# Performance work log

Hardware: AMD Instinct MI355X
Metric: run time of the kernel (lower is better)

The kernel has to match this reference:

```python
import jax, jax.numpy as jnp
import numpy as np

V, E, H = 32000, 256, 512
B, S, T = 32, 80, 80


def setup_inputs() -> dict:
    key = jax.random.key(0)
    ks = jax.random.split(key, 16)
    s = 0.05
    emb = jax.random.normal(ks[0], (V, E), jnp.float32) * s
    emb = emb.at[0].set(0.0)  # padding_idx=0 row is zero
    inp = {
        "src": jax.random.randint(ks[1], (B, S), 0, V),
        "tgt": jax.random.randint(ks[2], (B, T), 0, V),
        "emb": emb,
        "enc_Wih": jax.random.normal(ks[3], (3 * H, E), jnp.float32) * s,
        "enc_Whh": jax.random.normal(ks[4], (3 * H, H), jnp.float32) * s,
        "enc_bih": jax.random.normal(ks[5], (3 * H,), jnp.float32) * s,
        "enc_bhh": jax.random.normal(ks[6], (3 * H,), jnp.float32) * s,
        "dec_Wih": jax.random.normal(ks[7], (3 * H, E), jnp.float32) * s,
        "dec_Whh": jax.random.normal(ks[8], (3 * H, H), jnp.float32) * s,
        "dec_bih": jax.random.normal(ks[9], (3 * H,), jnp.float32) * s,
        "dec_bhh": jax.random.normal(ks[10], (3 * H,), jnp.float32) * s,
        "out_W": jax.random.normal(ks[11], (V, 2 * H), jnp.float32) * s,
        "out_b": jax.random.normal(ks[12], (V,), jnp.float32) * s,
    }
    return inp


def _gru_cell(x, h, Wih, Whh, bih, bhh):
    # PyTorch GRU cell: gates ordered (r, z, n)
    gi = x @ Wih.T + bih          # (B, 3H)
    gh = h @ Whh.T + bhh          # (B, 3H)
    i_r, i_z, i_n = jnp.split(gi, 3, axis=-1)
    h_r, h_z, h_n = jnp.split(gh, 3, axis=-1)
    r = jax.nn.sigmoid(i_r + h_r)
    z = jax.nn.sigmoid(i_z + h_z)
    n = jnp.tanh(i_n + r * h_n)
    return (1.0 - z) * n + z * h


def reference(src, tgt, emb, enc_Wih, enc_Whh, enc_bih, enc_bhh,
              dec_Wih, dec_Whh, dec_bih, dec_bhh, out_W, out_b):
    Bsz, Tlen = tgt.shape

    # ---- encoder: single-layer GRU over src ----
    x_src = emb[src]                              # (B, S, E)
    h0 = jnp.zeros((Bsz, H), x_src.dtype)

    def enc_step(h, x_t):
        h = _gru_cell(x_t, h, enc_Wih, enc_Whh, enc_bih, enc_bhh)
        return h, h

    h_enc, enc_outs = jax.lax.scan(enc_step, h0, jnp.swapaxes(x_src, 0, 1))
    enc_outs = jnp.swapaxes(enc_outs, 0, 1)       # (B, S, H)

    # ---- decoder: teacher forcing (ratio=1.0), steps t=1..T-1 ----
    x_dec = emb[tgt[:, :-1]]                      # (B, T-1, E)

    def dec_step(h, x_t):
        h = _gru_cell(x_t, h, dec_Wih, dec_Whh, dec_bih, dec_bhh)
        # Luong dot attention on new hidden state
        scores = jnp.einsum('bsh,bh->bs', enc_outs, h)
        aw = jax.nn.softmax(scores, axis=1)
        ctx = jnp.einsum('bs,bsh->bh', aw, enc_outs)
        combined = jnp.concatenate([h, ctx], axis=1)   # (B, 2H)
        step_logits = combined @ out_W.T + out_b       # (B, V)
        return h, step_logits

    _, step_logits = jax.lax.scan(dec_step, h_enc, jnp.swapaxes(x_dec, 0, 1))
    step_logits = jnp.swapaxes(step_logits, 0, 1)      # (B, T-1, V)

    # logits[:, 0, :] stays zero, matching the torch module
    logits = jnp.concatenate(
        [jnp.zeros((Bsz, 1, V), step_logits.dtype), step_logits], axis=1)
    return logits
```

## Files before the change

### kernel.cpp

```cpp
#include <hip/hip_runtime.h>

#define VV 32000
#define EE 256
#define HH 512
#define BB 32
#define SS 80
#define TT 80

typedef __attribute__((ext_vector_type(8))) _Float16 half8;
typedef __attribute__((ext_vector_type(4))) _Float16 half4;
typedef __attribute__((ext_vector_type(4))) float floatx4;
typedef unsigned long long u64;

__device__ __forceinline__ void gload16(const _Float16* g, _Float16* l) {
  __builtin_amdgcn_global_load_lds((const __attribute__((address_space(1))) void*)g,
                                   (__attribute__((address_space(3))) void*)l, 16, 0, 0);
}

__device__ __forceinline__ u64 aload(const u64* p) {
  return __hip_atomic_load(p, __ATOMIC_RELAXED, __HIP_MEMORY_SCOPE_AGENT);
}
__device__ __forceinline__ void astore(u64* p, u64 v) {
  __hip_atomic_store(p, v, __ATOMIC_RELAXED, __HIP_MEMORY_SCOPE_AGENT);
}

__device__ __forceinline__ unsigned pack15(unsigned short u) {
  return (u & 0x3FFFu) | ((u >> 1) & 0x4000u);
}
__device__ __forceinline__ unsigned short unpack15(unsigned v) {
  return (unsigned short)((v & 0x3FFFu) | ((v & 0x4000u) << 1));
}
__device__ __forceinline__ u64 unpack_word4(u64 a) {
  u64 o = 0;
#pragma unroll
  for (int i = 0; i < 4; ++i)
    o |= (u64)unpack15((unsigned)(a >> (15*i)) & 0x7FFFu) << (16*i);
  return o;
}

__device__ __forceinline__ float dot8(half8 a, half8 b, float c) {
  typedef __attribute__((ext_vector_type(2))) _Float16 half2v;
  half2v a0 = {a[0],a[1]}, a1 = {a[2],a[3]}, a2 = {a[4],a[5]}, a3 = {a[6],a[7]};
  half2v b0 = {b[0],b[1]}, b1 = {b[2],b[3]}, b2 = {b[4],b[5]}, b3 = {b[6],b[7]};
  c = __builtin_amdgcn_fdot2(a0, b0, c, false);
  c = __builtin_amdgcn_fdot2(a1, b1, c, false);
  c = __builtin_amdgcn_fdot2(a2, b2, c, false);
  c = __builtin_amdgcn_fdot2(a3, b3, c, false);
  return c;
}

__device__ __forceinline__ float sigm(float x) { return 1.f/(1.f + __expf(-x)); }
__device__ __forceinline__ float tanh_f(float x) { return 2.f/(1.f + __expf(-2.f*x)) - 1.f; }

__global__ __launch_bounds__(256) void giE_direct(
    const int* __restrict__ src, const float* __restrict__ emb,
    const float* __restrict__ Wih, const float* __restrict__ bih,
    float* __restrict__ gi)
{
  __shared__ _Float16 As[4096];
  __shared__ _Float16 Bs[4096];
  const int tid = threadIdx.x;
  const int lane = tid & 63;
  const int wv = tid >> 6;
  const int wr = wv >> 1, wc = wv & 1;
  const int mt = blockIdx.y, nt = blockIdx.x;
  floatx4 acc[4][4];
#pragma unroll
  for (int i=0;i<4;++i)
#pragma unroll
    for (int j=0;j<4;++j) acc[i][j] = (floatx4){0.f,0.f,0.f,0.f};
  const int r2 = tid >> 1, cb = (tid & 1) * 16;
  const int tok = src[mt*128 + r2];
  const float* arow = emb + (size_t)tok*EE;
  const float* brow = Wih + (size_t)(nt*128 + r2)*EE;
  const int g8 = (lane >> 4) * 8;
  const int lr = lane & 15;
  for (int kb = 0; kb < EE; kb += 32) {
    __syncthreads();
#pragma unroll
    for (int q = 0; q < 4; ++q) {
      const floatx4 va = *(const floatx4*)(arow + kb + cb + q*4);
      const floatx4 vb = *(const floatx4*)(brow + kb + cb + q*4);
#pragma unroll
      for (int e = 0; e < 4; ++e) {
        As[r2*32 + cb + q*4 + e] = (_Float16)va[e];
        Bs[r2*32 + cb + q*4 + e] = (_Float16)vb[e];
      }
    }
    __syncthreads();
    half8 af[4], bf[4];
#pragma unroll
    for (int i=0;i<4;++i) af[i] = *(const half8*)(As + (wr*64 + i*16 + lr)*32 + g8);
#pragma unroll
    for (int j=0;j<4;++j) bf[j] = *(const half8*)(Bs + (wc*64 + j*16 + lr)*32 + g8);
#pragma unroll
    for (int i=0;i<4;++i)
#pragma unroll
      for (int j=0;j<4;++j)
        acc[i][j] = __builtin_amdgcn_mfma_f32_16x16x32_f16(af[i], bf[j], acc[i][j], 0,0,0);
  }
  const int rm = 4*(lane>>4);
#pragma unroll
  for (int i=0;i<4;++i)
#pragma unroll
    for (int r=0;r<4;++r) {
      const int row = mt*128 + wr*64 + i*16 + rm + r;
#pragma unroll
      for (int j=0;j<4;++j) {
        const int col = nt*128 + wc*64 + j*16 + lr;
        gi[(size_t)row*1536 + col] = acc[i][j][r] + bih[col];
      }
    }
}

__global__ __launch_bounds__(256) void giD_direct(
    const int* __restrict__ tgt, const float* __restrict__ emb,
    const float* __restrict__ Wih, const float* __restrict__ bih,
    float* __restrict__ gi)
{
  __shared__ _Float16 As[4096];
  __shared__ _Float16 Bs[4096];
  const int tid = threadIdx.x;
  const int lane = tid & 63;
  const int wv = tid >> 6;
  const int wr = wv >> 1, wc = wv & 1;
  const int mt = blockIdx.y, nt = blockIdx.x;
  floatx4 acc[4][4];
#pragma unroll
  for (int i=0;i<4;++i)
#pragma unroll
    for (int j=0;j<4;++j) acc[i][j] = (floatx4){0.f,0.f,0.f,0.f};
  const int r2 = tid >> 1, cb = (tid & 1) * 16;
  const int R = mt*128 + r2;
  int tok = -1;
  if (R < 2528) { const int b_ = R/79, tt = R - b_*79; tok = tgt[b_*80 + tt]; }
  const float* arow = (tok >= 0) ? emb + (size_t)tok*EE : nullptr;
  const float* brow = Wih + (size_t)(nt*128 + r2)*EE;
  const int g8 = (lane >> 4) * 8;
  const int lr = lane & 15;
  for (int kb = 0; kb < EE; kb += 32) {
    __syncthreads();
    if (arow) {
#pragma unroll
      for (int q = 0; q < 4; ++q) {
        const floatx4 va = *(const floatx4*)(arow + kb + cb + q*4);
#pragma unroll
        for (int e = 0; e < 4; ++e) As[r2*32 + cb + q*4 + e] = (_Float16)va[e];
      }
    } else {
#pragma unroll
      for (int q = 0; q < 16; ++q) As[r2*32 + cb + q] = (_Float16)0.f;
    }
#pragma unroll
    for (int q = 0; q < 4; ++q) {
      const floatx4 vb = *(const floatx4*)(brow + kb + cb + q*4);
#pragma unroll
      for (int e = 0; e < 4; ++e) Bs[r2*32 + cb + q*4 + e] = (_Float16)vb[e];
    }
    __syncthreads();
    half8 af[4], bf[4];
#pragma unroll
    for (int i=0;i<4;++i) af[i] = *(const half8*)(As + (wr*64 + i*16 + lr)*32 + g8);
#pragma unroll
    for (int j=0;j<4;++j) bf[j] = *(const half8*)(Bs + (wc*64 + j*16 + lr)*32 + g8);
#pragma unroll
    for (int i=0;i<4;++i)
#pragma unroll
      for (int j=0;j<4;++j)
        acc[i][j] = __builtin_amdgcn_mfma_f32_16x16x32_f16(af[i], bf[j], acc[i][j], 0,0,0);
  }
  const int rm = 4*(lane>>4);
#pragma unroll
  for (int i=0;i<4;++i)
#pragma unroll
    for (int r=0;r<4;++r) {
      const int row = mt*128 + wv ? 0 : 0, dummy = 0; (void)dummy;
    }
#pragma unroll
  for (int i=0;i<4;++i)
#pragma unroll
    for (int r=0;r<4;++r) {
      const int row = mt*128 + wr*64 + i*16 + rm + r;
      if (row < 2528) {
#pragma unroll
        for (int j=0;j<4;++j) {
          const int col = nt*128 + wc*64 + j*16 + lr;
          gi[(size_t)row*1536 + col] = acc[i][j][r] + bih[col];
        }
      }
    }
}

__global__ __launch_bounds__(256) void oWh_conv(
    const float* __restrict__ ow, _Float16* __restrict__ owh)
{
  const long total8 = (long)VV*1024/8;
  for (long i = (long)blockIdx.x*256 + threadIdx.x; i < total8; i += (long)gridDim.x*256) {
    const float* s_ = ow + i*8;
    const floatx4 a = *(const floatx4*)s_;
    const floatx4 b = *(const floatx4*)(s_ + 4);
    half8 h;
    h[0]=(_Float16)a[0]; h[1]=(_Float16)a[1]; h[2]=(_Float16)a[2]; h[3]=(_Float16)a[3];
    h[4]=(_Float16)b[0]; h[5]=(_Float16)b[1]; h[6]=(_Float16)b[2]; h[7]=(_Float16)b[3];
    *(half8*)(owh + i*8) = h;
  }
}

__global__ __launch_bounds__(256) void logits_gemm(
    const _Float16* __restrict__ A, const _Float16* __restrict__ Bm,
    const float* __restrict__ bias, float* __restrict__ out)
{
  const int p = blockIdx.x;
  const int x = p & 7, s = p >> 3;
  const int nt = x + 8*(s / 20);
  const int mt = s % 20;
  if (nt >= 250) return;
  __shared__ _Float16 As[4096];
  __shared__ _Float16 Bs[4096];
  const int tid = threadIdx.x;
  const int lane = tid & 63;
  const int wv = tid >> 6;
  const int wr = wv >> 1, wc = wv & 1;
  floatx4 acc[4][4];
#pragma unroll
  for (int i=0;i<4;++i)
#pragma unroll
    for (int j=0;j<4;++j) acc[i][j] = (floatx4){0.f,0.f,0.f,0.f};
  const int srow = lane >> 2;
  const int scol = (lane & 3) * 8;
  const _Float16* Ab = A + (size_t)(mt*128)*1024;
  const _Float16* Bb = Bm + (size_t)(nt*128)*1024;
  const int g8 = (lane >> 4) * 8;
  const int lr = lane & 15;
  for (int kb = 0; kb < 1024; kb += 32) {
    __syncthreads();
#pragma unroll
    for (int cc = 0; cc < 2; ++cc) {
      const int c = wv*2 + cc;
      gload16(Ab + (size_t)(c*16 + srow)*1024 + kb + scol, As + c*512);
      gload16(Bb + (size_t)(c*16 + srow)*1024 + kb + scol, Bs + c*512);
    }
    __syncthreads();
    half8 af[4], bf[4];
#pragma unroll
    for (int i=0;i<4;++i) af[i] = *(const half8*)(As + (wr*64 + i*16 + lr)*32 + g8);
#pragma unroll
    for (int j=0;j<4;++j) bf[j] = *(const half8*)(Bs + (wc*64 + j*16 + lr)*32 + g8);
#pragma unroll
    for (int i=0;i<4;++i)
#pragma unroll
      for (int j=0;j<4;++j)
        acc[i][j] = __builtin_amdgcn_mfma_f32_16x16x32_f16(af[i], bf[j], acc[i][j], 0,0,0);
  }
  const int rm = 4*(lane>>4);
#pragma unroll
  for (int i=0;i<4;++i)
#pragma unroll
    for (int r=0;r<4;++r) {
      const int row = mt*128 + wr*64 + i*16 + rm + r;
#pragma unroll
      for (int j=0;j<4;++j) {
        const int col = nt*128 + wc*64 + j*16 + lr;
        if (row < 2528) {
          const int b = row / 79;
          const int t = row - b*79;
          out[(size_t)(b*80 + t + 1)*VV + col] = acc[i][j][r] + bias[col];
        } else {
          out[(size_t)((row - 2528)*80)*VV + col] = 0.f;
        }
      }
    }
}

#define SEQ_SMEM (80*512*2 + 512*2 + 512*2 + 3*64*8*4 + 2*80*4)
__global__ __launch_bounds__(512) void seq_pb(
    const float* __restrict__ eWhh, const float* __restrict__ dWhh,
    const float* __restrict__ ebhh, const float* __restrict__ dbhh,
    const float* __restrict__ giE, const float* __restrict__ giD,
    u64* __restrict__ hx,
    _Float16* __restrict__ comb)
{
  extern __shared__ char smem[];
  _Float16* eo_l = (_Float16*)smem;
  _Float16* hbuf = eo_l + 80*512;
  _Float16* hatt = hbuf + 512;
  float* part = (float*)(hatt + 512);
  float* sc = part + 3*64*8;
  float* aw = sc + 80;

  const int bi = blockIdx.x;
  const int q = bi >> 5, b = bi & 31;
  const int tid = threadIdx.x;
  const int lane = tid & 63;
  const int wv = tid >> 6;
  const int jl = tid & 63;
  const int kq = tid >> 6;
  const int j  = q*64 + jl;

  half8 wreg[3][8];
  auto loadW = [&](const float* W){
#pragma unroll
    for (int g = 0; g < 3; ++g)
#pragma unroll
      for (int c = 0; c < 8; ++c) {
        const float* s8 = W + ((size_t)(g*512 + j))*512 + kq*64 + c*8;
        const floatx4 a = *(const floatx4*)s8;
        const floatx4 d = *(const floatx4*)(s8 + 4);
        half8 h;
        h[0]=(_Float16)a[0]; h[1]=(_Float16)a[1]; h[2]=(_Float16)a[2]; h[3]=(_Float16)a[3];
        h[4]=(_Float16)d[0]; h[5]=(_Float16)d[1]; h[6]=(_Float16)d[2]; h[7]=(_Float16)d[3];
        wreg[g][c] = h;
      }
  };

  auto consume = [&](int slotR, u64 rtag){
    if (tid < 112) {
      const int m = tid + (tid >= q*16 ? 16 : 0);
      const u64* sp = hx + (size_t)slotR*4096 + b*128 + m;
      u64 v = aload(sp);
      int guard = 0;
      while ((v >> 60) != rtag && guard < (1<<22)) { v = aload(sp); ++guard; }
      *(u64*)&hbuf[m*4] = unpack_word4(v);
    }
    __syncthreads();
  };
  auto publish = [&](int slotW, u64 wtag){
    if (tid < 16) {
      const int m = q*16 + tid;
      u64 wq = wtag << 60;
#pragma unroll
      for (int e = 0; e < 4; ++e) {
        union { _Float16 h; unsigned short u; } cv; cv.h = hbuf[m*4 + e];
        wq |= (u64)pack15(cv.u) << (15*e);
      }
      astore(hx + (size_t)slotW*4096 + b*128 + m, wq);
    }
  };

  float hp = 0.f;
  auto gru = [&](float gr_, float gz_, float gn_, float bR, float bZ, float bN){
    half8 hv[8];
#pragma unroll
    for (int c = 0; c < 8; ++c) hv[c] = *(const half8*)&hbuf[kq*64 + c*8];
    float p0 = 0.f, p1 = 0.f, p2 = 0.f;
#pragma unroll
    for (int c = 0; c < 8; ++c) {
      p0 = dot8(wreg[0][c], hv[c], p0);
      p1 = dot8(wreg[1][c], hv[c], p1);
      p2 = dot8(wreg[2][c], hv[c], p2);
    }
    part[(0*64 + jl)*8 + kq] = p0;
    part[(1*64 + jl)*8 + kq] = p1;
    part[(2*64 + jl)*8 + kq] = p2;
    __syncthreads();
    if (tid < 64) {
      float a0 = 0.f, a1 = 0.f, a2 = 0.f;
#pragma unroll
      for (int e = 0; e < 8; ++e) {
        a0 += part[(0*64 + tid)*8 + e];
        a1 += part[(1*64 + tid)*8 + e];
        a2 += part[(2*64 + tid)*8 + e];
      }
      const float rg = sigm(gr_ + a0 + bR);
      const float zg = sigm(gz_ + a1 + bZ);
      const float ng = tanh_f(gn_ + rg*(a2 + bN));
      const float hn = (1.f - zg)*ng + zg*hp;
      hp = hn;
      hbuf[q*64 + tid] = (_Float16)hn;
    }
    __syncthreads();
  };

  auto attention = [&](int trow){
    const half8 hf = *(const half8*)&hatt[lane*8];
#pragma unroll 2
    for (int i = 0; i < 10; ++i) {
      const int s = wv*10 + i;
      const half8 ev = *(const half8*)&eo_l[s*512 + lane*8];
      float pt = dot8(ev, hf, 0.f);
#pragma unroll
      for (int o = 32; o; o >>= 1) pt += __shfl_xor(pt, o);
      if (lane == 0) sc[s] = pt;
    }
    __syncthreads();
    if (wv == 0) {
      const float v0 = sc[lane];
      const float v1 = (lane < 16) ? sc[64+lane] : -1e30f;
      float m = fmaxf(v0, v1);
#pragma unroll
      for (int o = 32; o; o >>= 1) m = fmaxf(m, __shfl_xor(m, o));
      const float e0 = __expf(v0 - m);
      const float e1 = (lane < 16) ? __expf(v1 - m) : 0.f;
      float ssum = e0 + e1;
#pragma unroll
      for (int o = 32; o; o >>= 1) ssum += __shfl_xor(ssum, o);
      const float inv = 1.f/ssum;
      aw[lane] = e0*inv;
      if (lane < 16) aw[64+lane] = e1*inv;
    }
    __syncthreads();
    if (tid < 64) {
      float c = 0.f;
#pragma unroll 8
      for (int s = 0; s < SS; ++s) c += aw[s] * (float)eo_l[s*512 + q*64 + tid];
      _Float16* cr = comb + ((size_t)b*79 + trow)*1024;
      cr[q*64 + tid]       = hatt[q*64 + tid];
      cr[512 + q*64 + tid] = (_Float16)c;
    }
    __syncthreads();
  };

  if (tid < 128) *(u64*)&hbuf[tid*4] = 0ull;
  loadW(eWhh);
  float ebR=0.f, ebZ=0.f, ebN=0.f, dbR=0.f, dbZ=0.f, dbN=0.f;
  if (tid < 64) {
    ebR = ebhh[j]; ebZ = ebhh[512+j]; ebN = ebhh[1024+j];
    dbR = dbhh[j]; dbZ = dbhh[512+j]; dbN = dbhh[1024+j];
  }
  __syncthreads();

  for (int k = 0; k < SS; ++k) {
    float gr_=0.f, gz_=0.f, gn_=0.f;
    if (tid < 64) {
      const float* gi = giE + ((size_t)b*SS + k)*1536;
      gr_ = gi[j]; gz_ = gi[512+j]; gn_ = gi[1024+j];
    }
    consume(k & 1, (u64)(k & 15));
    if (k > 0 && tid < 128)
      *(u64*)&eo_l[(k-1)*512 + tid*4] = *(const u64*)&hbuf[tid*4];
    gru(gr_, gz_, gn_, ebR, ebZ, ebN);
    publish((k+1) & 1, (u64)((k+1) & 15));
  }

  loadW(dWhh);

  for (int t = 0; t < TT-1; ++t) {
    const int k = 80 + t;
    float gr_=0.f, gz_=0.f, gn_=0.f;
    if (tid < 64) {
      const float* gi = giD + ((size_t)b*79 + t)*1536;
      gr_ = gi[j]; gz_ = gi[512+j]; gn_ = gi[1024+j];
    }
    consume(k & 1, (u64)(k & 15));
    if (tid < 128) {
      if (t == 0) *(u64*)&eo_l[79*512 + tid*4] = *(const u64*)&hbuf[tid*4];
      else        *(u64*)&hatt[tid*4]          = *(const u64*)&hbuf[tid*4];
    }
    gru(gr_, gz_, gn_, dbR, dbZ, dbN);
    publish((k+1) & 1, (u64)((k+1) & 15));
    if (t > 0) attention(t-1);
  }

  if (tid < 112) {
    const int m = tid + (tid >= q*16 ? 16 : 0);
    const u64* sp = hx + (size_t)4096 + b*128 + m;
    u64 v = aload(sp);
    int guard = 0;
    while ((v >> 60) != 15ull && guard < (1<<22)) { v = aload(sp); ++guard; }
    *(u64*)&hbuf[m*4] = unpack_word4(v);
  }
  __syncthreads();
  if (tid < 128) *(u64*)&hatt[tid*4] = *(const u64*)&hbuf[tid*4];
  __syncthreads();
  attention(TT-2);
}

extern "C" void kernel_launch(void* const* d_in, const int* in_sizes, int n_in,
                              void* d_out, int out_size, void* d_ws, size_t ws_size,
                              hipStream_t stream) {
  (void)in_sizes; (void)n_in; (void)out_size; (void)ws_size;
  const int*   src  = (const int*)d_in[0];
  const int*   tgt  = (const int*)d_in[1];
  const float* emb  = (const float*)d_in[2];
  const float* eWih = (const float*)d_in[3];
  const float* eWhh = (const float*)d_in[4];
  const float* ebih = (const float*)d_in[5];
  const float* ebhh = (const float*)d_in[6];
  const float* dWih = (const float*)d_in[7];
  const float* dWhh = (const float*)d_in[8];
  const float* dbih = (const float*)d_in[9];
  const float* dbhh = (const float*)d_in[10];
  const float* outW = (const float*)d_in[11];
  const float* outb = (const float*)d_in[12];
  float* out = (float*)d_out;

  char* p = (char*)d_ws;
  auto alloc = [&](size_t n){ char* r = p; p += (n + 255) & ~(size_t)255; return r; };
  _Float16* oWh  = (_Float16*)alloc((size_t)VV*1024*2);
  float*    giE  = (float*)alloc((size_t)2560*1536*4);
  float*    giD  = (float*)alloc((size_t)2560*1536*4);
  u64*      hx   = (u64*)alloc((size_t)2*32*128*8);
  _Float16* comb = (_Float16*)alloc((size_t)2560*1024*2);

  hipMemsetAsync(hx, 0, (size_t)2*32*128*8, stream);
  giE_direct<<<dim3(12,20), 256, 0, stream>>>(src, emb, eWih, ebih, giE);
  giD_direct<<<dim3(12,20), 256, 0, stream>>>(tgt, emb, dWih, dbih, giD);
  oWh_conv<<<1024, 256, 0, stream>>>(outW, oWh);
  hipFuncSetAttribute((const void*)seq_pb,
                      hipFuncAttributeMaxDynamicSharedMemorySize, SEQ_SMEM);
  seq_pb<<<256, 512, SEQ_SMEM, stream>>>(eWhh, dWhh, ebhh, dbhh, giE, giD,
                                         hx, comb);
  logits_gemm<<<5120, 256, 0, stream>>>(comb, oWh, outb, out);
}
```

Measured before the change: 986.7 us.

## Fuse input-gate GEMMs and convert output weights to fp16 inside logits GEMM

Merges the encoder and decoder input-projection GEMMs into one launch with a 24x20 grid, and removes the separate fp32-to-fp16 conversion pass over the output weight matrix. The logits GEMM now loads fp32 weight rows directly and converts them into shared memory, so the 64MB-read and 64MB-write conversion pass is gone. The cost is that each logits tile reads fp32 weights, which doubles B-operand traffic across the 20 M-tiles that reuse each weight tile. It also drops the async global-to-LDS load for the B operand in favour of a register staging path.

```diff
diff --git a/kernel.cpp b/kernel.cpp
--- a/kernel.cpp
+++ b/kernel.cpp
@@ -52,10 +52,12 @@
 __device__ __forceinline__ float sigm(float x) { return 1.f/(1.f + __expf(-x)); }
 __device__ __forceinline__ float tanh_f(float x) { return 2.f/(1.f + __expf(-2.f*x)) - 1.f; }
 
-__global__ __launch_bounds__(256) void giE_direct(
-    const int* __restrict__ src, const float* __restrict__ emb,
-    const float* __restrict__ Wih, const float* __restrict__ bih,
-    float* __restrict__ gi)
+__global__ __launch_bounds__(256) void gi_fused(
+    const int* __restrict__ src, const int* __restrict__ tgt,
+    const float* __restrict__ emb,
+    const float* __restrict__ eWih, const float* __restrict__ ebih,
+    const float* __restrict__ dWih, const float* __restrict__ dbih,
+    float* __restrict__ giE, float* __restrict__ giD)
 {
   __shared__ _Float16 As[4096];
   __shared__ _Float16 Bs[4096];
@@ -63,68 +65,12 @@
   const int lane = tid & 63;
   const int wv = tid >> 6;
   const int wr = wv >> 1, wc = wv & 1;
-  const int mt = blockIdx.y, nt = blockIdx.x;
-  floatx4 acc[4][4];
-#pragma unroll
-  for (int i=0;i<4;++i)
-#pragma unroll
-    for (int j=0;j<4;++j) acc[i][j] = (floatx4){0.f,0.f,0.f,0.f};
-  const int r2 = tid >> 1, cb = (tid & 1) * 16;
-  const int tok = src[mt*128 + r2];
-  const float* arow = emb + (size_t)tok*EE;
-  const float* brow = Wih + (size_t)(nt*128 + r2)*EE;
-  const int g8 = (lane >> 4) * 8;
-  const int lr = lane & 15;
-  for (int kb = 0; kb < EE; kb += 32) {
-    __syncthreads();
-#pragma unroll
-    for (int q = 0; q < 4; ++q) {
-      const floatx4 va = *(const floatx4*)(arow + kb + cb + q*4);
-      const floatx4 vb = *(const floatx4*)(brow + kb + cb + q*4);
-#pragma unroll
-      for (int e = 0; e < 4; ++e) {
-        As[r2*32 + cb + q*4 + e] = (_Float16)va[e];
-        Bs[r2*32 + cb + q*4 + e] = (_Float16)vb[e];
-      }
-    }
-    __syncthreads();
-    half8 af[4], bf[4];
-#pragma unroll
-    for (int i=0;i<4;++i) af[i] = *(const half8*)(As + (wr*64 + i*16 + lr)*32 + g8);
-#pragma unroll
-    for (int j=0;j<4;++j) bf[j] = *(const half8*)(Bs + (wc*64 + j*16 + lr)*32 + g8);
-#pragma unroll
-    for (int i=0;i<4;++i)
-#pragma unroll
-      for (int j=0;j<4;++j)
-        acc[i][j] = __builtin_amdgcn_mfma_f32_16x16x32_f16(af[i], bf[j], acc[i][j], 0,0,0);
-  }
-  const int rm = 4*(lane>>4);
-#pragma unroll
-  for (int i=0;i<4;++i)
-#pragma unroll
-    for (int r=0;r<4;++r) {
-      const int row = mt*128 + wr*64 + i*16 + rm + r;
-#pragma unroll
-      for (int j=0;j<4;++j) {
-        const int col = nt*128 + wc*64 + j*16 + lr;
-        gi[(size_t)row*1536 + col] = acc[i][j][r] + bih[col];
-      }
-    }
-}
-
-__global__ __launch_bounds__(256) void giD_direct(
-    const int* __restrict__ tgt, const float* __restrict__ emb,
-    const float* __restrict__ Wih, const float* __restrict__ bih,
-    float* __restrict__ gi)
-{
-  __shared__ _Float16 As[4096];
-  __shared__ _Float16 Bs[4096];
-  const int tid = threadIdx.x;
-  const int lane = tid & 63;
-  const int wv = tid >> 6;
-  const int wr = wv >> 1, wc = wv & 1;
-  const int mt = blockIdx.y, nt = blockIdx.x;
+  const int mt = blockIdx.y;
+  const bool isE = blockIdx.x < 12;
+  const int nt = isE ? blockIdx.x : blockIdx.x - 12;
+  const float* Wih = isE ? eWih : dWih;
+  const float* bih = isE ? ebih : dbih;
+  float* gi = isE ? giE : giD;
   floatx4 acc[4][4];
 #pragma unroll
   for (int i=0;i<4;++i)
@@ -133,7 +79,8 @@
   const int r2 = tid >> 1, cb = (tid & 1) * 16;
   const int R = mt*128 + r2;
   int tok = -1;
-  if (R < 2528) { const int b_ = R/79, tt = R - b_*79; tok = tgt[b_*80 + tt]; }
+  if (isE) tok = src[R];
+  else if (R < 2528) { const int b_ = R/79, tt = R - b_*79; tok = tgt[b_*80 + tt]; }
   const float* arow = (tok >= 0) ? emb + (size_t)tok*EE : nullptr;
   const float* brow = Wih + (size_t)(nt*128 + r2)*EE;
   const int g8 = (lane >> 4) * 8;
@@ -174,14 +121,8 @@
   for (int i=0;i<4;++i)
 #pragma unroll
     for (int r=0;r<4;++r) {
-      const int row = mt*128 + wv ? 0 : 0, dummy = 0; (void)dummy;
-    }
-#pragma unroll
-  for (int i=0;i<4;++i)
-#pragma unroll
-    for (int r=0;r<4;++r) {
       const int row = mt*128 + wr*64 + i*16 + rm + r;
-      if (row < 2528) {
+      if (isE || row < 2528) {
 #pragma unroll
         for (int j=0;j<4;++j) {
           const int col = nt*128 + wc*64 + j*16 + lr;
@@ -191,23 +132,9 @@
     }
 }
 
-__global__ __launch_bounds__(256) void oWh_conv(
-    const float* __restrict__ ow, _Float16* __restrict__ owh)
-{
-  const long total8 = (long)VV*1024/8;
-  for (long i = (long)blockIdx.x*256 + threadIdx.x; i < total8; i += (long)gridDim.x*256) {
-    const float* s_ = ow + i*8;
-    const floatx4 a = *(const floatx4*)s_;
-    const floatx4 b = *(const floatx4*)(s_ + 4);
-    half8 h;
-    h[0]=(_Float16)a[0]; h[1]=(_Float16)a[1]; h[2]=(_Float16)a[2]; h[3]=(_Float16)a[3];
-    h[4]=(_Float16)b[0]; h[5]=(_Float16)b[1]; h[6]=(_Float16)b[2]; h[7]=(_Float16)b[3];
-    *(half8*)(owh + i*8) = h;
-  }
-}
-
 __global__ __launch_bounds__(256) void logits_gemm(
-    const _Float16* __restrict__ A, const _Float16* __restrict__ Bm,
+    const _Float16* __restrict__ A,
+    const float* __restrict__ Bw,
     const float* __restrict__ bias, float* __restrict__ out)
 {
   const int p = blockIdx.x;
@@ -229,7 +156,8 @@
   const int srow = lane >> 2;
   const int scol = (lane & 3) * 8;
   const _Float16* Ab = A + (size_t)(mt*128)*1024;
-  const _Float16* Bb = Bm + (size_t)(nt*128)*1024;
+  const int r2 = tid >> 1, cb = (tid & 1) * 16;
+  const float* brow = Bw + (size_t)(nt*128 + r2)*1024;
   const int g8 = (lane >> 4) * 8;
   const int lr = lane & 15;
   for (int kb = 0; kb < 1024; kb += 32) {
@@ -238,7 +166,12 @@
     for (int cc = 0; cc < 2; ++cc) {
       const int c = wv*2 + cc;
       gload16(Ab + (size_t)(c*16 + srow)*1024 + kb + scol, As + c*512);
-      gload16(Bb + (size_t)(c*16 + srow)*1024 + kb + scol, Bs + c*512);
+    }
+#pragma unroll
+    for (int q = 0; q < 4; ++q) {
+      const floatx4 vb = *(const floatx4*)(brow + kb + cb + q*4);
+#pragma unroll
+      for (int e = 0; e < 4; ++e) Bs[r2*32 + cb + q*4 + e] = (_Float16)vb[e];
     }
     __syncthreads();
     half8 af[4], bf[4];
@@ -486,19 +419,17 @@
 
   char* p = (char*)d_ws;
   auto alloc = [&](size_t n){ char* r = p; p += (n + 255) & ~(size_t)255; return r; };
-  _Float16* oWh  = (_Float16*)alloc((size_t)VV*1024*2);
   float*    giE  = (float*)alloc((size_t)2560*1536*4);
   float*    giD  = (float*)alloc((size_t)2560*1536*4);
   u64*      hx   = (u64*)alloc((size_t)2*32*128*8);
   _Float16* comb = (_Float16*)alloc((size_t)2560*1024*2);
 
   hipMemsetAsync(hx, 0, (size_t)2*32*128*8, stream);
-  giE_direct<<<dim3(12,20), 256, 0, stream>>>(src, emb, eWih, ebih, giE);
-  giD_direct<<<dim3(12,20), 256, 0, stream>>>(tgt, emb, dWih, dbih, giD);
-  oWh_conv<<<1024, 256, 0, stream>>>(outW, oWh);
+  gi_fused<<<dim3(24,20), 256, 0, stream>>>(src, tgt, emb, eWih, ebih,
+                                            dWih, dbih, giE, giD);
   hipFuncSetAttribute((const void*)seq_pb,
                       hipFuncAttributeMaxDynamicSharedMemorySize, SEQ_SMEM);
   seq_pb<<<256, 512, SEQ_SMEM, stream>>>(eWhh, dWhh, ebhh, dbhh, giE, giD,
                                          hx, comb);
-  logits_gemm<<<5120, 256, 0, stream>>>(comb, oWh, outb, out);
-}
+  logits_gemm<<<5120, 256, 0, stream>>>(comb, outW, outb, out);
+}
```

Measured after the change: 1.083 ms. 9.8% more time.
